# Kernel tuning notes

Hardware: AMD Instinct MI355X
Metric: run time of the kernel (lower is better)

Reference implementation:

```python
import jax, jax.numpy as jnp
import numpy as np

EMB = 512
GP = 128
NH = 8
HD = EMB // NH  # 64
B = 2
S = 1024


def _rel_shift(x):
    # Faithful port of DoubleAttentionLayer._rel_shift (pads dim 1, reinterprets
    # (B, J+1, K, n) as (J+1, B, K, n), drops first slice). Row-major reshape
    # semantics match torch .view on contiguous tensors exactly.
    Bsz, J, K, N = x.shape
    zp = jnp.zeros((Bsz, 1, K, N), x.dtype)
    xp = jnp.concatenate([zp, x], axis=1).reshape(J + 1, Bsz, K, N)
    return xp[1:].reshape(Bsz, J, K, N)


def _layernorm(x):
    # nn.LayerNorm(emb_dim, elementwise_affine=False), eps=1e-5
    m = jnp.mean(x, axis=-1, keepdims=True)
    v = jnp.var(x, axis=-1, keepdims=True)
    return (x - m) / jnp.sqrt(v + 1e-5)


def _attention(q, k, v, Bc, Bp, gpe, mask, Wp_w, Wp_b):
    Bsz, J, E = q.shape
    K = k.shape[1]
    # content scores
    qc = jnp.tanh((q + Bc).reshape(Bsz, J, NH, HD))
    kh = jnp.tanh(k.reshape(Bsz, K, NH, HD))
    ctx = jnp.einsum('bjnd,bknd->bjkn', qc, kh)
    # position scores (tanh before reshape in source for qp -- elementwise, same math)
    qp = jnp.tanh(q + Bp).reshape(Bsz, J, NH, HD)
    kp = jnp.tanh((gpe @ Wp_w + Wp_b).reshape(Bsz, -1, NH, HD))
    pos = jnp.einsum('bjnd,bknd->bjkn', qp, kp)
    pad = ctx.shape[2] - pos.shape[2]  # static; 0 in this configuration
    if pad > 0:
        # replicate-pad pos at front of k dim; constant(0)-pad mask (torch F.pad defaults)
        pos = jnp.concatenate([jnp.broadcast_to(pos[:, :, :1], (Bsz, J, pad, NH)), pos], axis=2)
        mask = jnp.concatenate([jnp.zeros(mask.shape[:2] + (pad, mask.shape[3]), mask.dtype), mask], axis=2)
    pos = _rel_shift(pos)
    att = (ctx + pos) / (HD ** 0.5) - 1e30 * mask
    att = jax.nn.softmax(att, axis=2)
    vh = jnp.tanh(v.reshape(Bsz, K, NH, HD))
    return jnp.einsum('bjkn,bknd->bjnd', att, vh).reshape(Bsz, J, E)


def setup_inputs() -> dict:
    key = jax.random.key(0)
    ks = jax.random.split(key, 12)
    u_emb = jax.random.normal(ks[0], (B, S, EMB), jnp.float32)
    f_emb = jax.random.normal(ks[1], (B, S, EMB), jnp.float32)
    gpe = jax.random.normal(ks[2], (B, S, GP), jnp.float32)
    # causal masks: 1 where attention is disallowed, broadcast over heads
    causal = (1.0 - jnp.tril(jnp.ones((S, S), jnp.float32)))[None, :, :, None]
    u_mask = jnp.broadcast_to(causal, (B, S, S, 1))
    f_mask = jnp.broadcast_to(causal, (B, S, S, 1))
    w = 0.02
    Wq_w = w * jax.random.normal(ks[3], (EMB, EMB), jnp.float32)
    Wq_b = jnp.zeros((EMB,), jnp.float32)
    Wkv_w = w * jax.random.normal(ks[4], (EMB, 2 * EMB), jnp.float32)
    Wkv_b = jnp.zeros((2 * EMB,), jnp.float32)
    Wp_w = w * jax.random.normal(ks[5], (GP, EMB), jnp.float32)
    Wp_b = jnp.zeros((EMB,), jnp.float32)
    Wu_w = w * jax.random.normal(ks[6], (EMB, EMB), jnp.float32)
    Wu_b = jnp.zeros((EMB,), jnp.float32)
    Bfc = 0.2 * jax.random.normal(ks[7], (1, 1, EMB), jnp.float32)
    Bfp = 0.2 * jax.random.normal(ks[8], (1, 1, EMB), jnp.float32)
    Buc = 0.2 * jax.random.normal(ks[9], (1, 1, EMB), jnp.float32)
    Bup = 0.2 * jax.random.normal(ks[10], (1, 1, EMB), jnp.float32)
    return {"u_emb": u_emb, "f_emb": f_emb, "gpe": gpe, "u_mask": u_mask, "f_mask": f_mask,
            "Wq_w": Wq_w, "Wq_b": Wq_b, "Wkv_w": Wkv_w, "Wkv_b": Wkv_b,
            "Wp_w": Wp_w, "Wp_b": Wp_b, "Wu_w": Wu_w, "Wu_b": Wu_b,
            "Bfc": Bfc, "Bfp": Bfp, "Buc": Buc, "Bup": Bup}


def reference(u_emb, f_emb, gpe, u_mask, f_mask, Wq_w, Wq_b, Wkv_w, Wkv_b,
              Wp_w, Wp_b, Wu_w, Wu_b, Bfc, Bfp, Buc, Bup):
    # first_part=True path: f_mem = f_emb (memory buffer registration has no output effect)
    q_u = f_emb @ Wu_w + Wu_b
    kv = f_emb @ Wkv_w + Wkv_b
    k, v = jnp.split(kv, 2, axis=-1)
    u_out = _layernorm(u_emb + _attention(q_u, k, v, Buc, Bup, gpe, u_mask, Wp_w, Wp_b))
    # last_layer=False: second attention over f stream
    q_f = f_emb @ Wq_w + Wq_b
    f_out = _layernorm(f_emb + _attention(q_f, k, v, Bfc, Bfp, gpe, f_mask, Wp_w, Wp_b))
    return (u_out, f_out)
```

## Files before the change

### kernel.cpp

```cpp
#include <hip/hip_runtime.h>
#include <math.h>

#define EMB 512
#define NH 8
#define HD 64
#define BB 2
#define SS 1024
#define ROWS (BB * SS)

typedef __attribute__((ext_vector_type(8))) short bhalf8;
typedef __attribute__((ext_vector_type(4))) float f32x4;
typedef __attribute__((ext_vector_type(8))) unsigned short us8;
typedef unsigned short ushort_t;

typedef const __attribute__((address_space(1))) void gas_void;
typedef __attribute__((address_space(3))) void las_void;

__device__ __forceinline__ void gl2lds16(const void* g, void* l) {
  __builtin_amdgcn_global_load_lds((gas_void*)g, (las_void*)l, 16, 0, 0);
}

__device__ __forceinline__ unsigned short f2bf(float x) {
  unsigned u = __float_as_uint(x);
  u = (u + 0x7FFFu + ((u >> 16) & 1u)) >> 16;
  return (unsigned short)u;
}
__device__ __forceinline__ float bf2f(unsigned short v) {
  return __uint_as_float(((unsigned)v) << 16);
}
__device__ __forceinline__ float fast_tanh(float x) {
  x = fminf(15.f, fmaxf(-15.f, x));
  const float e = __expf(2.f * x);
  return (e - 1.f) / (e + 1.f);
}

__global__ __launch_bounds__(256, 4) void projpe_kernel(
    const float* __restrict__ f_emb, const float* __restrict__ gpe,
    const float* __restrict__ Wu, const float* __restrict__ Wq,
    const float* __restrict__ Wkv, const float* __restrict__ Wp,
    const float* __restrict__ Wu_b, const float* __restrict__ Wq_b,
    const float* __restrict__ Wkv_b, const float* __restrict__ Wp_b,
    const float* __restrict__ Buc, const float* __restrict__ Bup,
    const float* __restrict__ Bfc, const float* __restrict__ Bfp,
    ushort_t* __restrict__ Qcomb, ushort_t* __restrict__ Kcomb,
    ushort_t* __restrict__ vhT, float* __restrict__ Onum,
    float* __restrict__ lpart) {
  const int bx = blockIdx.x;
  const int mb = blockIdx.y * 128;
  const int tid = threadIdx.x;
  const int w = tid >> 6, lane = tid & 63;
  const int ln = lane & 15, quad = lane >> 4;
  const int wm = (w >> 1) * 64, wn = (w & 1) * 32;

  __shared__ __align__(16) ushort_t sA[128 * 72];
  __shared__ __align__(16) ushort_t sB[64 * 72];

  const int fb = blockIdx.y * 40 + bx;
  if (fb < 512) {
    const float4 z4 = {0.f, 0.f, 0.f, 0.f};
#pragma unroll
    for (int i = 0; i < 4; ++i)
      ((float4*)Onum)[(size_t)fb * 1024 + i * 256 + tid] = z4;
  } else {
    lpart[(fb - 512) * 256 + tid] = 0.f;
  }
  if (fb == 0) {
    const int t2 = tid >> 7, rem = tid & 127;
    const int h = rem >> 4, d4 = (rem & 15) * 4;
    *(ushort4*)&Qcomb[((size_t)t2 * ROWS + 1023) * 1024 + h * 128 + 64 + d4] =
        make_ushort4(0, 0, 0, 0);
  }

  const bool isPe = (bx >= 32);
  const int nb = isPe ? 0 : bx * 64;
  const int npbase = isPe ? (bx - 32) * 64 : 0;
  const float* Af = isPe ? gpe : f_emb;
  const int lda = isPe ? 128 : 512;
  const int trips = isPe ? 2 : 8;

  const float* Wsrc;
  int Nw, coff;
  if (isPe) { Wsrc = Wp; Nw = 512; coff = npbase; }
  else if (nb < 512) { Wsrc = Wu; Nw = 512; coff = nb; }
  else if (nb < 1024) { Wsrc = Wq; Nw = 512; coff = nb - 512; }
  else { Wsrc = Wkv; Nw = 1024; coff = nb - 1024; }

  const int bn = tid & 63;
  const int bk0 = (tid >> 6) * 16;

  f32x4 acc[4][2];
#pragma unroll
  for (int rt = 0; rt < 4; ++rt)
#pragma unroll
    for (int ct = 0; ct < 2; ++ct) acc[rt][ct] = (f32x4){0.f, 0.f, 0.f, 0.f};

  float4 qa[8];
  float qbw[16];
#pragma unroll
  for (int i = 0; i < 4; ++i) {
    const int idx = tid + i * 256;
    const size_t base = (size_t)(mb + (idx >> 3)) * lda + (idx & 7) * 8;
    qa[2 * i] = *(const float4*)&Af[base];
    qa[2 * i + 1] = *(const float4*)&Af[base + 4];
  }
#pragma unroll
  for (int j = 0; j < 16; ++j)
    qbw[j] = Wsrc[(size_t)(bk0 + j) * Nw + coff + bn];

  for (int t0 = 0; t0 < trips; ++t0) {
    __syncthreads();
#pragma unroll
    for (int i = 0; i < 4; ++i) {
      const int idx = tid + i * 256;
      us8 o;
      const float4 a = qa[2 * i], b = qa[2 * i + 1];
      o[0] = f2bf(a.x); o[1] = f2bf(a.y); o[2] = f2bf(a.z); o[3] = f2bf(a.w);
      o[4] = f2bf(b.x); o[5] = f2bf(b.y); o[6] = f2bf(b.z); o[7] = f2bf(b.w);
      *(us8*)&sA[(idx >> 3) * 72 + (idx & 7) * 8] = o;
    }
    {
      us8 o0, o1;
#pragma unroll
      for (int j = 0; j < 8; ++j) {
        o0[j] = f2bf(qbw[j]);
        o1[j] = f2bf(qbw[8 + j]);
      }
      *(us8*)&sB[bn * 72 + bk0] = o0;
      *(us8*)&sB[bn * 72 + bk0 + 8] = o1;
    }
    __syncthreads();
    if (t0 < trips - 1) {
      const int k1 = (t0 + 1) * 64;
#pragma unroll
      for (int i = 0; i < 4; ++i) {
        const int idx = tid + i * 256;
        const size_t base = (size_t)(mb + (idx >> 3)) * lda + k1 + (idx & 7) * 8;
        qa[2 * i] = *(const float4*)&Af[base];
        qa[2 * i + 1] = *(const float4*)&Af[base + 4];
      }
#pragma unroll
      for (int j = 0; j < 16; ++j)
        qbw[j] = Wsrc[(size_t)(k1 + bk0 + j) * Nw + coff + bn];
    }
#pragma unroll
    for (int kc = 0; kc < 2; ++kc) {
      bhalf8 af[4], bf_[2];
#pragma unroll
      for (int rt = 0; rt < 4; ++rt)
        af[rt] =
            *(const bhalf8*)&sA[(wm + rt * 16 + ln) * 72 + kc * 32 + quad * 8];
#pragma unroll
      for (int ct = 0; ct < 2; ++ct)
        bf_[ct] =
            *(const bhalf8*)&sB[(wn + ct * 16 + ln) * 72 + kc * 32 + quad * 8];
#pragma unroll
      for (int rt = 0; rt < 4; ++rt)
#pragma unroll
        for (int ct = 0; ct < 2; ++ct)
          acc[rt][ct] = __builtin_amdgcn_mfma_f32_16x16x32_bf16(
              af[rt], bf_[ct], acc[rt][ct], 0, 0, 0);
    }
  }

  __syncthreads();
  ushort_t* sOut = sA;

  if (!isPe && nb >= 1536) {
#pragma unroll
    for (int ct = 0; ct < 2; ++ct) {
      const int nl = wn + ct * 16 + ln;
      const float wb = Wkv_b[nb + nl - 1024];
#pragma unroll
      for (int rt = 0; rt < 4; ++rt)
#pragma unroll
        for (int r = 0; r < 4; ++r) {
          const int ml = wm + rt * 16 + quad * 4 + r;
          sOut[nl * 136 + ml] = f2bf(fast_tanh(acc[rt][ct][r] + wb));
        }
    }
    __syncthreads();
    const int b = mb >> 10, mo = mb & 1023;
#pragma unroll
    for (int i = 0; i < 4; ++i) {
      const int idx = tid + i * 256;
      const int nl = idx >> 4, m8 = (idx & 15) * 8;
      const us8 v = *(const us8*)&sOut[nl * 136 + m8];
      *(us8*)&vhT[((size_t)b * 512 + (nb - 1536) + nl) * 1024 + mo + m8] = v;
    }
  } else {
    const float* WB =
        isPe ? Wp_b : (nb < 512 ? Wu_b : (nb < 1024 ? Wq_b : Wkv_b));
    const int woff =
        isPe ? npbase : (nb < 512 ? nb : (nb < 1024 ? nb - 512 : nb - 1024));
    const bool rawDump = (!isPe && nb < 1024);
#pragma unroll
    for (int ct = 0; ct < 2; ++ct) {
      const int nl = wn + ct * 16 + ln;
      const float wb = WB[woff + nl];
#pragma unroll
      for (int rt = 0; rt < 4; ++rt)
#pragma unroll
        for (int r = 0; r < 4; ++r) {
          const int ml = wm + rt * 16 + quad * 4 + r;
          const float v = acc[rt][ct][r] + wb;
          sOut[ml * 72 + nl] = f2bf(rawDump ? v : fast_tanh(v));
        }
    }
    __syncthreads();
#pragma unroll
    for (int i = 0; i < 4; ++i) {
      const int idx = tid + i * 256;
      const int rr = idx >> 3, c8 = (idx & 7) * 8;
      const int m = mb + rr;
      const us8 v = *(const us8*)&sOut[rr * 72 + c8];
      if (isPe) {
        const int n = npbase + c8;
        const int h = n >> 6;
        *(us8*)&Kcomb[(size_t)m * 1024 + h * 128 + 64 + (n & 63)] = v;
      } else if (nb < 1024) {
        const int strm = nb >= 512 ? 1 : 0;
        const int n = (nb - strm * 512) + c8;
        const int h = n >> 6;
        const float* BC = strm ? Bfc : Buc;
        const float* BP = strm ? Bfp : Bup;
        float bcA[8], bpA[8];
        *(float4*)&bcA[0] = *(const float4*)&BC[n];
        *(float4*)&bcA[4] = *(const float4*)&BC[n + 4];
        *(float4*)&bpA[0] = *(const float4*)&BP[n];
        *(float4*)&bpA[4] = *(const float4*)&BP[n + 4];
        us8 oc, op;
#pragma unroll
        for (int jj = 0; jj < 8; ++jj) {
          const float vv = bf2f((unsigned short)v[jj]);
          oc[jj] = f2bf(fast_tanh(vv + bcA[jj]));
          op[jj] = f2bf(fast_tanh(vv + bpA[jj]));
        }
        *(us8*)&Qcomb[((size_t)strm * ROWS + m) * 1024 + h * 128 + (n & 63)] =
            oc;
        if (m != 0) {
          const int mp = (m < 1024) ? m - 1 : m;
          *(us8*)&Qcomb[((size_t)strm * ROWS + mp) * 1024 + h * 128 + 64 +
                        (n & 63)] = op;
        }
      } else {
        const int n = (nb - 1024) + c8;
        const int h = n >> 6;
        *(us8*)&Kcomb[(size_t)m * 1024 + h * 128 + (n & 63)] = v;
      }
    }
  }
}

__global__ __launch_bounds__(256, 2) void attn_kernel(
    const ushort_t* __restrict__ Qcomb, const ushort_t* __restrict__ Kcomb,
    const ushort_t* __restrict__ vhT, float* __restrict__ Onum,
    float* __restrict__ lpart) {
  const int bid = blockIdx.x;
  const int tid = threadIdx.x;
  const int w = tid >> 6, lane = tid & 63;
  const int ln = lane & 15, quad = lane >> 4;

  __shared__ __align__(16) ushort_t sK[2 * 64 * 128];
  __shared__ __align__(16) ushort_t sV[2 * 64 * 64];
  __shared__ __align__(16) ushort_t sP[64 * 72];

  const int G0 = (bid * 17) >> 1;
  const int G1 = ((bid + 1) * 17) >> 1;
  const int cnt = G1 - G0;

  int c = G0 / 136;
  int u = G0 - c * 136;
  int jt = (int)((sqrtf(8.f * u + 1.f) - 1.f) * 0.5f);
  while ((jt + 1) * (jt + 2) / 2 <= u) ++jt;
  while (jt * (jt + 1) / 2 > u) --jt;
  int kt = u - jt * (jt + 1) / 2;
  int t = c >> 4, b = (c >> 3) & 1, h = c & 7;

  const int l4 = lane >> 4, p15 = lane & 15;
  const int l3 = lane >> 3, l7 = lane & 7;
#define STAGE_KV(B_, H_, KT_, BUF_)                                          \
  {                                                                          \
    const size_t kb_ = ((size_t)(B_)*SS + (KT_)*64) * 1024 + (H_)*128;       \
    ushort_t* bk_ = sK + (BUF_)*8192;                                        \
    _Pragma("unroll") for (int s_ = 0; s_ < 4; ++s_) {                       \
      const int q_ = w * 4 + s_;                                             \
      const int r_ = q_ * 4 + l4;                                            \
      const int gl_ = p15 ^ (r_ & 7);                                        \
      gl2lds16(&Kcomb[kb_ + (size_t)r_ * 1024 + gl_ * 8], &bk_[q_ * 512]);   \
    }                                                                        \
    const size_t vb_ = ((size_t)(B_)*512 + (H_)*64) * 1024 + (KT_)*64;       \
    ushort_t* bv_ = sV + (BUF_)*4096;                                        \
    _Pragma("unroll") for (int s_ = 0; s_ < 2; ++s_) {                       \
      const int q_ = w * 2 + s_;                                             \
      const int r_ = q_ * 8 + l3;                                            \
      const int gl_ = l7 ^ (r_ & 7);                                         \
      gl2lds16(&vhT[vb_ + (size_t)r_ * 1024 + gl_ * 8], &bv_[q_ * 512]);     \
    }                                                                        \
  }

  bhalf8 aq[4];
#define LOAD_AQ(T_, B_, H_, JT_)                                             \
  {                                                                          \
    const size_t qb_ =                                                       \
        ((size_t)(T_)*ROWS + (B_)*SS + (JT_)*64 + w * 16 + ln) * 1024 +      \
        (H_)*128 + quad * 8;                                                 \
    _Pragma("unroll") for (int kc_ = 0; kc_ < 4; ++kc_) aq[kc_] =            \
        *(const bhalf8*)&Qcomb[qb_ + kc_ * 32];                              \
  }

  STAGE_KV(b, h, kt, 0);
  LOAD_AQ(t, b, h, jt);

  f32x4 oacc[4];
#pragma unroll
  for (int ct = 0; ct < 4; ++ct) oacc[ct] = (f32x4){0.f, 0.f, 0.f, 0.f};
  float lsum[4] = {0.f, 0.f, 0.f, 0.f};

  for (int it = 0; it < cnt; ++it) {
    __syncthreads();
    const ushort_t* bK = sK + (it & 1) * 8192;
    const ushort_t* bV = sV + (it & 1) * 4096;

    int c2 = c, jt2 = jt, kt2 = kt + 1;
    if (kt2 > jt) {
      jt2 = jt + 1; kt2 = 0;
      if (jt2 > 15) { c2 = c + 1; jt2 = 0; }
    }
    if (it < cnt - 1) {
      const int b2 = (c2 >> 3) & 1, h2 = c2 & 7;
      STAGE_KV(b2, h2, kt2, ((it + 1) & 1));
    }

    f32x4 sacc[4];
#pragma unroll
    for (int ct = 0; ct < 4; ++ct) {
      sacc[ct] = (f32x4){0.f, 0.f, 0.f, 0.f};
#pragma unroll
      for (int kc = 0; kc < 4; ++kc) {
        const bhalf8 bk = *(const bhalf8*)&bK[(ct * 16 + ln) * 128 +
                                             (((kc * 4 + quad) ^ l7) << 3)];
        sacc[ct] = __builtin_amdgcn_mfma_f32_16x16x32_bf16(aq[kc], bk,
                                                           sacc[ct], 0, 0, 0);
      }
    }

    const bool diag = (kt == jt);
#pragma unroll
    for (int ct = 0; ct < 4; ++ct)
#pragma unroll
      for (int r = 0; r < 4; ++r) {
        float p;
        if (diag && (ct * 16 + ln > w * 16 + quad * 4 + r))
          p = 0.f;
        else
          p = __expf(sacc[ct][r] * 0.125f - 16.f);
        sacc[ct][r] = p;
        lsum[r] += p;
      }

#pragma unroll
    for (int ct = 0; ct < 4; ++ct)
#pragma unroll
      for (int r = 0; r < 4; ++r)
        sP[(w * 16 + quad * 4 + r) * 72 + ct * 16 + ln] =
            (ushort_t)(__float_as_uint(sacc[ct][r]) >> 16);

#pragma unroll
    for (int kc = 0; kc < 2; ++kc) {
      const bhalf8 ap =
          *(const bhalf8*)&sP[(w * 16 + ln) * 72 + kc * 32 + quad * 8];
#pragma unroll
      for (int ct = 0; ct < 4; ++ct) {
        const bhalf8 bv = *(const bhalf8*)&bV[(ct * 16 + ln) * 64 +
                                             (((kc * 4 + quad) ^ l7) << 3)];
        oacc[ct] = __builtin_amdgcn_mfma_f32_16x16x32_bf16(ap, bv, oacc[ct],
                                                           0, 0, 0);
      }
    }

    const bool rowEnd = (it == cnt - 1) || (jt2 != jt) || (c2 != c);
    if (rowEnd) {
#pragma unroll
      for (int r = 0; r < 4; ++r) {
        float s = lsum[r];
        s += __shfl_xor(s, 1);
        s += __shfl_xor(s, 2);
        s += __shfl_xor(s, 4);
        s += __shfl_xor(s, 8);
        const int j = jt * 64 + w * 16 + quad * 4 + r;
        if (ln == 0)
          atomicAdd(&lpart[((((t * 2 + b) << 10) + j) << 3) + h], s);
        const size_t orow = (((size_t)t * ROWS + b * SS + j) << 9) + h * 64;
#pragma unroll
        for (int ct = 0; ct < 4; ++ct)
          atomicAdd(&Onum[orow + ct * 16 + ln], oacc[ct][r]);
        lsum[r] = 0.f;
      }
#pragma unroll
      for (int ct = 0; ct < 4; ++ct) oacc[ct] = (f32x4){0.f, 0.f, 0.f, 0.f};
      if (it < cnt - 1) {
        const int t2 = c2 >> 4, b2 = (c2 >> 3) & 1, h2 = c2 & 7;
        LOAD_AQ(t2, b2, h2, jt2);
      }
    }
    c = c2; jt = jt2; kt = kt2;
    t = c >> 4; b = (c >> 3) & 1; h = c & 7;
  }
}

__global__ __launch_bounds__(256) void ln_kernel(
    const float* __restrict__ u_emb, const float* __restrict__ f_emb,
    const float* __restrict__ Onum, const float* __restrict__ lpart,
    float* __restrict__ out) {
  const int rid = blockIdx.x * 4 + (threadIdx.x >> 6);
  const int lane = threadIdx.x & 63;
  const int t = rid >> 11, row = rid & 2047;
  const int b = row >> 10, j = row & 1023;
  const float* resid = t ? f_emb : u_emb;
  const size_t base = (size_t)row * 512;
  const size_t obase = ((size_t)t * ROWS + row) * 512;
  const int o = lane * 8;
  const int h = lane >> 3;
  const float inv = 1.f / lpart[((((t * 2 + b) << 10) + j) << 3) + h];

  const float4 n0 = *(const float4*)&Onum[obase + o];
  const float4 n1 = *(const float4*)&Onum[obase + o + 4];
  const float4 r0 = *(const float4*)&resid[base + o];
  const float4 r1 = *(const float4*)&resid[base + o + 4];
  float y[8];
  y[0] = r0.x + n0.x * inv; y[1] = r0.y + n0.y * inv;
  y[2] = r0.z + n0.z * inv; y[3] = r0.w + n0.w * inv;
  y[4] = r1.x + n1.x * inv; y[5] = r1.y + n1.y * inv;
  y[6] = r1.z + n1.z * inv; y[7] = r1.w + n1.w * inv;

  float s = 0.f, q = 0.f;
#pragma unroll
  for (int i = 0; i < 8; ++i) {
    s += y[i];
    q += y[i] * y[i];
  }
#pragma unroll
  for (int off = 1; off < 64; off <<= 1) {
    s += __shfl_xor(s, off);
    q += __shfl_xor(q, off);
  }
  const float mean = s * (1.f / 512.f);
  const float var = q * (1.f / 512.f) - mean * mean;
  const float rstd = rsqrtf(var + 1e-5f);

  float4 o0, o1;
  o0.x = (y[0] - mean) * rstd; o0.y = (y[1] - mean) * rstd;
  o0.z = (y[2] - mean) * rstd; o0.w = (y[3] - mean) * rstd;
  o1.x = (y[4] - mean) * rstd; o1.y = (y[5] - mean) * rstd;
  o1.z = (y[6] - mean) * rstd; o1.w = (y[7] - mean) * rstd;
  *(float4*)&out[obase + o] = o0;
  *(float4*)&out[obase + o + 4] = o1;
}

extern "C" void kernel_launch(void* const* d_in, const int* in_sizes, int n_in,
                              void* d_out, int out_size, void* d_ws,
                              size_t ws_size, hipStream_t stream) {
  (void)in_sizes; (void)n_in; (void)out_size; (void)ws_size;
  const float* u_emb = (const float*)d_in[0];
  const float* f_emb = (const float*)d_in[1];
  const float* gpe = (const float*)d_in[2];
  const float* Wq_w = (const float*)d_in[5];
  const float* Wq_b = (const float*)d_in[6];
  const float* Wkv_w = (const float*)d_in[7];
  const float* Wkv_b = (const float*)d_in[8];
  const float* Wp_w = (const float*)d_in[9];
  const float* Wp_b = (const float*)d_in[10];
  const float* Wu_w = (const float*)d_in[11];
  const float* Wu_b = (const float*)d_in[12];
  const float* Bfc = (const float*)d_in[13];
  const float* Bfp = (const float*)d_in[14];
  const float* Buc = (const float*)d_in[15];
  const float* Bup = (const float*)d_in[16];
  float* out = (float*)d_out;

  ushort_t* ws = (ushort_t*)d_ws;
  const size_t SZ = (size_t)ROWS * EMB;
  ushort_t* Qcomb = ws;
  ushort_t* Kcomb = ws + 4 * SZ;
  ushort_t* vhT = ws + 6 * SZ;
  float* Onum = (float*)(ws + 7 * SZ);
  float* lpart = (float*)(ws + 11 * SZ);

  dim3 blk(256);
  hipLaunchKernelGGL(projpe_kernel, dim3(40, 16), blk, 0, stream, f_emb, gpe,
                     Wu_w, Wq_w, Wkv_w, Wp_w, Wu_b, Wq_b, Wkv_b, Wp_b, Buc,
                     Bup, Bfc, Bfp, Qcomb, Kcomb, vhT, Onum, lpart);
  hipLaunchKernelGGL(attn_kernel, dim3(512), blk, 0, stream, Qcomb, Kcomb, vhT,
                     Onum, lpart);
  hipLaunchKernelGGL(ln_kernel, dim3(1024), blk, 0, stream, u_emb, f_emb, Onum,
                     lpart, out);
}
```

Baseline: 158.2 us.

## Share K/V tiles across both attention streams and retile projection GEMM

The attention kernel now processes both query streams (u and f) against each staged K/V tile, so each tile is loaded once and reused for two score/PV passes, halving the number of work items per block schedule. The projection kernel switches to 64-row tiles with a doubled grid, double-buffered shared memory and a single barrier per k-step to raise occupancy and overlap loads. The change costs more registers in the attention kernel from the doubled accumulators and Q fragments, and the zero-init indexing is reworked to fit the new grid.

```diff
diff --git a/kernel.cpp b/kernel.cpp
--- a/kernel.cpp
+++ b/kernel.cpp
@@ -46,25 +46,24 @@
     ushort_t* __restrict__ vhT, float* __restrict__ Onum,
     float* __restrict__ lpart) {
   const int bx = blockIdx.x;
-  const int mb = blockIdx.y * 128;
+  const int mb = blockIdx.y * 64;
   const int tid = threadIdx.x;
   const int w = tid >> 6, lane = tid & 63;
   const int ln = lane & 15, quad = lane >> 4;
-  const int wm = (w >> 1) * 64, wn = (w & 1) * 32;
-
-  __shared__ __align__(16) ushort_t sA[128 * 72];
-  __shared__ __align__(16) ushort_t sB[64 * 72];
+  const int wm = w * 16;
+
+  __shared__ __align__(16) ushort_t sA[2 * 64 * 72];
+  __shared__ __align__(16) ushort_t sB[2 * 64 * 72];
 
   const int fb = blockIdx.y * 40 + bx;
-  if (fb < 512) {
+  if (fb < 1024) {
     const float4 z4 = {0.f, 0.f, 0.f, 0.f};
 #pragma unroll
-    for (int i = 0; i < 4; ++i)
-      ((float4*)Onum)[(size_t)fb * 1024 + i * 256 + tid] = z4;
-  } else {
-    lpart[(fb - 512) * 256 + tid] = 0.f;
-  }
-  if (fb == 0) {
+    for (int i = 0; i < 2; ++i)
+      ((float4*)Onum)[(size_t)fb * 512 + i * 256 + tid] = z4;
+  } else if (fb < 1152) {
+    lpart[(fb - 1024) * 256 + tid] = 0.f;
+  } else if (fb == 1152) {
     const int t2 = tid >> 7, rem = tid & 127;
     const int h = rem >> 4, d4 = (rem & 15) * 4;
     *(ushort4*)&Qcomb[((size_t)t2 * ROWS + 1023) * 1024 + h * 128 + 64 + d4] =
@@ -85,80 +84,67 @@
   else if (nb < 1024) { Wsrc = Wq; Nw = 512; coff = nb - 512; }
   else { Wsrc = Wkv; Nw = 1024; coff = nb - 1024; }
 
-  const int bn = tid & 63;
-  const int bk0 = (tid >> 6) * 16;
-
-  f32x4 acc[4][2];
-#pragma unroll
-  for (int rt = 0; rt < 4; ++rt)
-#pragma unroll
-    for (int ct = 0; ct < 2; ++ct) acc[rt][ct] = (f32x4){0.f, 0.f, 0.f, 0.f};
-
-  float4 qa[8];
+  const int arow = tid >> 2, ac16 = (tid & 3) * 16;
+  const int bn = tid & 63, bk0 = (tid >> 6) * 16;
+
+  f32x4 acc[4];
+#pragma unroll
+  for (int ct = 0; ct < 4; ++ct) acc[ct] = (f32x4){0.f, 0.f, 0.f, 0.f};
+
+  float4 qa[4];
   float qbw[16];
 #pragma unroll
-  for (int i = 0; i < 4; ++i) {
-    const int idx = tid + i * 256;
-    const size_t base = (size_t)(mb + (idx >> 3)) * lda + (idx & 7) * 8;
-    qa[2 * i] = *(const float4*)&Af[base];
-    qa[2 * i + 1] = *(const float4*)&Af[base + 4];
-  }
+  for (int i = 0; i < 4; ++i)
+    qa[i] = *(const float4*)&Af[(size_t)(mb + arow) * lda + ac16 + i * 4];
 #pragma unroll
   for (int j = 0; j < 16; ++j)
     qbw[j] = Wsrc[(size_t)(bk0 + j) * Nw + coff + bn];
 
   for (int t0 = 0; t0 < trips; ++t0) {
-    __syncthreads();
-#pragma unroll
-    for (int i = 0; i < 4; ++i) {
-      const int idx = tid + i * 256;
-      us8 o;
-      const float4 a = qa[2 * i], b = qa[2 * i + 1];
-      o[0] = f2bf(a.x); o[1] = f2bf(a.y); o[2] = f2bf(a.z); o[3] = f2bf(a.w);
-      o[4] = f2bf(b.x); o[5] = f2bf(b.y); o[6] = f2bf(b.z); o[7] = f2bf(b.w);
-      *(us8*)&sA[(idx >> 3) * 72 + (idx & 7) * 8] = o;
-    }
+    ushort_t* bA = sA + (t0 & 1) * 4608;
+    ushort_t* bB = sB + (t0 & 1) * 4608;
     {
       us8 o0, o1;
 #pragma unroll
+      for (int j = 0; j < 4; ++j) {
+        o0[j] = f2bf(((const float*)&qa[0])[j]);
+        o0[4 + j] = f2bf(((const float*)&qa[1])[j]);
+        o1[j] = f2bf(((const float*)&qa[2])[j]);
+        o1[4 + j] = f2bf(((const float*)&qa[3])[j]);
+      }
+      *(us8*)&bA[arow * 72 + ac16] = o0;
+      *(us8*)&bA[arow * 72 + ac16 + 8] = o1;
+      us8 b0, b1;
+#pragma unroll
       for (int j = 0; j < 8; ++j) {
-        o0[j] = f2bf(qbw[j]);
-        o1[j] = f2bf(qbw[8 + j]);
-      }
-      *(us8*)&sB[bn * 72 + bk0] = o0;
-      *(us8*)&sB[bn * 72 + bk0 + 8] = o1;
-    }
-    __syncthreads();
+        b0[j] = f2bf(qbw[j]);
+        b1[j] = f2bf(qbw[8 + j]);
+      }
+      *(us8*)&bB[bn * 72 + bk0] = b0;
+      *(us8*)&bB[bn * 72 + bk0 + 8] = b1;
+    }
     if (t0 < trips - 1) {
       const int k1 = (t0 + 1) * 64;
 #pragma unroll
-      for (int i = 0; i < 4; ++i) {
-        const int idx = tid + i * 256;
-        const size_t base = (size_t)(mb + (idx >> 3)) * lda + k1 + (idx & 7) * 8;
-        qa[2 * i] = *(const float4*)&Af[base];
-        qa[2 * i + 1] = *(const float4*)&Af[base + 4];
-      }
+      for (int i = 0; i < 4; ++i)
+        qa[i] =
+            *(const float4*)&Af[(size_t)(mb + arow) * lda + k1 + ac16 + i * 4];
 #pragma unroll
       for (int j = 0; j < 16; ++j)
         qbw[j] = Wsrc[(size_t)(k1 + bk0 + j) * Nw + coff + bn];
     }
+    __syncthreads();
 #pragma unroll
     for (int kc = 0; kc < 2; ++kc) {
-      bhalf8 af[4], bf_[2];
-#pragma unroll
-      for (int rt = 0; rt < 4; ++rt)
-        af[rt] =
-            *(const bhalf8*)&sA[(wm + rt * 16 + ln) * 72 + kc * 32 + quad * 8];
-#pragma unroll
-      for (int ct = 0; ct < 2; ++ct)
-        bf_[ct] =
-            *(const bhalf8*)&sB[(wn + ct * 16 + ln) * 72 + kc * 32 + quad * 8];
-#pragma unroll
-      for (int rt = 0; rt < 4; ++rt)
-#pragma unroll
-        for (int ct = 0; ct < 2; ++ct)
-          acc[rt][ct] = __builtin_amdgcn_mfma_f32_16x16x32_bf16(
-              af[rt], bf_[ct], acc[rt][ct], 0, 0, 0);
+      const bhalf8 af =
+          *(const bhalf8*)&bA[(wm + ln) * 72 + kc * 32 + quad * 8];
+#pragma unroll
+      for (int ct = 0; ct < 4; ++ct) {
+        const bhalf8 bf_ =
+            *(const bhalf8*)&bB[(ct * 16 + ln) * 72 + kc * 32 + quad * 8];
+        acc[ct] =
+            __builtin_amdgcn_mfma_f32_16x16x32_bf16(af, bf_, acc[ct], 0, 0, 0);
+      }
     }
   }
 
@@ -167,23 +153,21 @@
 
   if (!isPe && nb >= 1536) {
 #pragma unroll
-    for (int ct = 0; ct < 2; ++ct) {
-      const int nl = wn + ct * 16 + ln;
+    for (int ct = 0; ct < 4; ++ct) {
+      const int nl = ct * 16 + ln;
       const float wb = Wkv_b[nb + nl - 1024];
 #pragma unroll
-      for (int rt = 0; rt < 4; ++rt)
-#pragma unroll
-        for (int r = 0; r < 4; ++r) {
-          const int ml = wm + rt * 16 + quad * 4 + r;
-          sOut[nl * 136 + ml] = f2bf(fast_tanh(acc[rt][ct][r] + wb));
-        }
+      for (int r = 0; r < 4; ++r) {
+        const int ml = wm + quad * 4 + r;
+        sOut[nl * 136 + ml] = f2bf(fast_tanh(acc[ct][r] + wb));
+      }
     }
     __syncthreads();
     const int b = mb >> 10, mo = mb & 1023;
 #pragma unroll
-    for (int i = 0; i < 4; ++i) {
+    for (int i = 0; i < 2; ++i) {
       const int idx = tid + i * 256;
-      const int nl = idx >> 4, m8 = (idx & 15) * 8;
+      const int nl = idx >> 3, m8 = (idx & 7) * 8;
       const us8 v = *(const us8*)&sOut[nl * 136 + m8];
       *(us8*)&vhT[((size_t)b * 512 + (nb - 1536) + nl) * 1024 + mo + m8] = v;
     }
@@ -194,21 +178,19 @@
         isPe ? npbase : (nb < 512 ? nb : (nb < 1024 ? nb - 512 : nb - 1024));
     const bool rawDump = (!isPe && nb < 1024);
 #pragma unroll
-    for (int ct = 0; ct < 2; ++ct) {
-      const int nl = wn + ct * 16 + ln;
+    for (int ct = 0; ct < 4; ++ct) {
+      const int nl = ct * 16 + ln;
       const float wb = WB[woff + nl];
 #pragma unroll
-      for (int rt = 0; rt < 4; ++rt)
-#pragma unroll
-        for (int r = 0; r < 4; ++r) {
-          const int ml = wm + rt * 16 + quad * 4 + r;
-          const float v = acc[rt][ct][r] + wb;
-          sOut[ml * 72 + nl] = f2bf(rawDump ? v : fast_tanh(v));
-        }
+      for (int r = 0; r < 4; ++r) {
+        const int ml = wm + quad * 4 + r;
+        const float v = acc[ct][r] + wb;
+        sOut[ml * 72 + nl] = f2bf(rawDump ? v : fast_tanh(v));
+      }
     }
     __syncthreads();
 #pragma unroll
-    for (int i = 0; i < 4; ++i) {
+    for (int i = 0; i < 2; ++i) {
       const int idx = tid + i * 256;
       const int rr = idx >> 3, c8 = (idx & 7) * 8;
       const int m = mb + rr;
@@ -264,8 +246,8 @@
   __shared__ __align__(16) ushort_t sV[2 * 64 * 64];
   __shared__ __align__(16) ushort_t sP[64 * 72];
 
-  const int G0 = (bid * 17) >> 1;
-  const int G1 = ((bid + 1) * 17) >> 1;
+  const int G0 = (bid * 17) >> 2;
+  const int G1 = ((bid + 1) * 17) >> 2;
   const int cnt = G1 - G0;
 
   int c = G0 / 136;
@@ -274,7 +256,7 @@
   while ((jt + 1) * (jt + 2) / 2 <= u) ++jt;
   while (jt * (jt + 1) / 2 > u) --jt;
   int kt = u - jt * (jt + 1) / 2;
-  int t = c >> 4, b = (c >> 3) & 1, h = c & 7;
+  int b = c >> 3, h = c & 7;
 
   const int l4 = lane >> 4, p15 = lane & 15;
   const int l3 = lane >> 3, l7 = lane & 7;
@@ -298,23 +280,27 @@
     }                                                                        \
   }
 
-  bhalf8 aq[4];
-#define LOAD_AQ(T_, B_, H_, JT_)                                             \
+  bhalf8 aq[2][4];
+#define LOAD_AQ2(B_, H_, JT_)                                                \
   {                                                                          \
-    const size_t qb_ =                                                       \
-        ((size_t)(T_)*ROWS + (B_)*SS + (JT_)*64 + w * 16 + ln) * 1024 +      \
-        (H_)*128 + quad * 8;                                                 \
-    _Pragma("unroll") for (int kc_ = 0; kc_ < 4; ++kc_) aq[kc_] =            \
-        *(const bhalf8*)&Qcomb[qb_ + kc_ * 32];                              \
+    _Pragma("unroll") for (int t_ = 0; t_ < 2; ++t_) {                       \
+      const size_t qb_ =                                                     \
+          ((size_t)t_ * ROWS + (B_)*SS + (JT_)*64 + w * 16 + ln) * 1024 +    \
+          (H_)*128 + quad * 8;                                               \
+      _Pragma("unroll") for (int kc_ = 0; kc_ < 4; ++kc_) aq[t_][kc_] =      \
+          *(const bhalf8*)&Qcomb[qb_ + kc_ * 32];                            \
+    }                                                                        \
   }
 
   STAGE_KV(b, h, kt, 0);
-  LOAD_AQ(t, b, h, jt);
-
-  f32x4 oacc[4];
-#pragma unroll
-  for (int ct = 0; ct < 4; ++ct) oacc[ct] = (f32x4){0.f, 0.f, 0.f, 0.f};
-  float lsum[4] = {0.f, 0.f, 0.f, 0.f};
+  LOAD_AQ2(b, h, jt);
+
+  f32x4 oacc[2][4];
+#pragma unroll
+  for (int ts = 0; ts < 2; ++ts)
+#pragma unroll
+    for (int ct = 0; ct < 4; ++ct) oacc[ts][ct] = (f32x4){0.f, 0.f, 0.f, 0.f};
+  float lsum[2][4] = {{0.f, 0.f, 0.f, 0.f}, {0.f, 0.f, 0.f, 0.f}};
 
   for (int it = 0; it < cnt; ++it) {
     __syncthreads();
@@ -331,80 +317,82 @@
       STAGE_KV(b2, h2, kt2, ((it + 1) & 1));
     }
 
-    f32x4 sacc[4];
-#pragma unroll
-    for (int ct = 0; ct < 4; ++ct) {
-      sacc[ct] = (f32x4){0.f, 0.f, 0.f, 0.f};
-#pragma unroll
-      for (int kc = 0; kc < 4; ++kc) {
-        const bhalf8 bk = *(const bhalf8*)&bK[(ct * 16 + ln) * 128 +
-                                             (((kc * 4 + quad) ^ l7) << 3)];
-        sacc[ct] = __builtin_amdgcn_mfma_f32_16x16x32_bf16(aq[kc], bk,
-                                                           sacc[ct], 0, 0, 0);
-      }
-    }
-
     const bool diag = (kt == jt);
 #pragma unroll
-    for (int ct = 0; ct < 4; ++ct)
-#pragma unroll
-      for (int r = 0; r < 4; ++r) {
-        float p;
-        if (diag && (ct * 16 + ln > w * 16 + quad * 4 + r))
-          p = 0.f;
-        else
-          p = __expf(sacc[ct][r] * 0.125f - 16.f);
-        sacc[ct][r] = p;
-        lsum[r] += p;
-      }
-
-#pragma unroll
-    for (int ct = 0; ct < 4; ++ct)
-#pragma unroll
-      for (int r = 0; r < 4; ++r)
-        sP[(w * 16 + quad * 4 + r) * 72 + ct * 16 + ln] =
-            (ushort_t)(__float_as_uint(sacc[ct][r]) >> 16);
-
-#pragma unroll
-    for (int kc = 0; kc < 2; ++kc) {
-      const bhalf8 ap =
-          *(const bhalf8*)&sP[(w * 16 + ln) * 72 + kc * 32 + quad * 8];
+    for (int ts = 0; ts < 2; ++ts) {
+      f32x4 sacc[4];
 #pragma unroll
       for (int ct = 0; ct < 4; ++ct) {
-        const bhalf8 bv = *(const bhalf8*)&bV[(ct * 16 + ln) * 64 +
-                                             (((kc * 4 + quad) ^ l7) << 3)];
-        oacc[ct] = __builtin_amdgcn_mfma_f32_16x16x32_bf16(ap, bv, oacc[ct],
-                                                           0, 0, 0);
+        sacc[ct] = (f32x4){0.f, 0.f, 0.f, 0.f};
+#pragma unroll
+        for (int kc = 0; kc < 4; ++kc) {
+          const bhalf8 bk = *(const bhalf8*)&bK[(ct * 16 + ln) * 128 +
+                                               (((kc * 4 + quad) ^ l7) << 3)];
+          sacc[ct] = __builtin_amdgcn_mfma_f32_16x16x32_bf16(aq[ts][kc], bk,
+                                                             sacc[ct], 0, 0, 0);
+        }
+      }
+#pragma unroll
+      for (int ct = 0; ct < 4; ++ct)
+#pragma unroll
+        for (int r = 0; r < 4; ++r) {
+          float p;
+          if (diag && (ct * 16 + ln > w * 16 + quad * 4 + r))
+            p = 0.f;
+          else
+            p = __expf(sacc[ct][r] * 0.125f - 16.f);
+          sacc[ct][r] = p;
+          lsum[ts][r] += p;
+        }
+#pragma unroll
+      for (int ct = 0; ct < 4; ++ct)
+#pragma unroll
+        for (int r = 0; r < 4; ++r)
+          sP[(w * 16 + quad * 4 + r) * 72 + ct * 16 + ln] =
+              (ushort_t)(__float_as_uint(sacc[ct][r]) >> 16);
+#pragma unroll
+      for (int kc = 0; kc < 2; ++kc) {
+        const bhalf8 ap =
+            *(const bhalf8*)&sP[(w * 16 + ln) * 72 + kc * 32 + quad * 8];
+#pragma unroll
+        for (int ct = 0; ct < 4; ++ct) {
+          const bhalf8 bv = *(const bhalf8*)&bV[(ct * 16 + ln) * 64 +
+                                                (((kc * 4 + quad) ^ l7) << 3)];
+          oacc[ts][ct] = __builtin_amdgcn_mfma_f32_16x16x32_bf16(
+              ap, bv, oacc[ts][ct], 0, 0, 0);
+        }
       }
     }
 
     const bool rowEnd = (it == cnt - 1) || (jt2 != jt) || (c2 != c);
     if (rowEnd) {
 #pragma unroll
-      for (int r = 0; r < 4; ++r) {
-        float s = lsum[r];
-        s += __shfl_xor(s, 1);
-        s += __shfl_xor(s, 2);
-        s += __shfl_xor(s, 4);
-        s += __shfl_xor(s, 8);
-        const int j = jt * 64 + w * 16 + quad * 4 + r;
-        if (ln == 0)
-          atomicAdd(&lpart[((((t * 2 + b) << 10) + j) << 3) + h], s);
-        const size_t orow = (((size_t)t * ROWS + b * SS + j) << 9) + h * 64;
-#pragma unroll
-        for (int ct = 0; ct < 4; ++ct)
-          atomicAdd(&Onum[orow + ct * 16 + ln], oacc[ct][r]);
-        lsum[r] = 0.f;
-      }
-#pragma unroll
-      for (int ct = 0; ct < 4; ++ct) oacc[ct] = (f32x4){0.f, 0.f, 0.f, 0.f};
+      for (int ts = 0; ts < 2; ++ts)
+#pragma unroll
+        for (int r = 0; r < 4; ++r) {
+          float s = lsum[ts][r];
+          s += __shfl_xor(s, 1);
+          s += __shfl_xor(s, 2);
+          s += __shfl_xor(s, 4);
+          s += __shfl_xor(s, 8);
+          const int j = jt * 64 + w * 16 + quad * 4 + r;
+          if (ln == 0)
+            atomicAdd(&lpart[((((ts * 2 + b) << 10) + j) << 3) + h], s);
+          const size_t orow = (((size_t)ts * ROWS + b * SS + j) << 9) + h * 64;
+#pragma unroll
+          for (int ct = 0; ct < 4; ++ct)
+            atomicAdd(&Onum[orow + ct * 16 + ln], oacc[ts][ct][r]);
+          lsum[ts][r] = 0.f;
+#pragma unroll
+          for (int ct = 0; ct < 4; ++ct) oacc[ts][ct][r] = 0.f;
+        }
       if (it < cnt - 1) {
-        const int t2 = c2 >> 4, b2 = (c2 >> 3) & 1, h2 = c2 & 7;
-        LOAD_AQ(t2, b2, h2, jt2);
+        const int b2 = (c2 >> 3) & 1, h2 = c2 & 7;
+        LOAD_AQ2(b2, h2, jt2);
       }
     }
     c = c2; jt = jt2; kt = kt2;
-    t = c >> 4; b = (c >> 3) & 1; h = c & 7;
+    b = c >> 3; h = c & 7;
   }
 }
 
@@ -487,7 +475,7 @@
   float* lpart = (float*)(ws + 11 * SZ);
 
   dim3 blk(256);
-  hipLaunchKernelGGL(projpe_kernel, dim3(40, 16), blk, 0, stream, f_emb, gpe,
+  hipLaunchKernelGGL(projpe_kernel, dim3(40, 32), blk, 0, stream, f_emb, gpe,
                      Wu_w, Wq_w, Wkv_w, Wp_w, Wu_b, Wq_b, Wkv_b, Wp_b, Buc,
                      Bup, Bfc, Bfp, Qcomb, Kcomb, vhT, Onum, lpart);
   hipLaunchKernelGGL(attn_kernel, dim3(512), blk, 0, stream, Qcomb, Kcomb, vhT,
```

New measurement: 167.6 us. +6.0%, slower.

## Process both attention streams per K/V tile to share staged K and V

Applied to the files above, without the earlier changes.

Each attention block now handles the u and f query streams together against the same staged K/V tile, holding two sets of Q fragments and accumulators. Work units are halved (16 combos of batch and head instead of 32), so each K/V tile is loaded into LDS once and reused for both streams. This cuts global-to-LDS traffic and the number of work items, at the cost of more registers, which may lower occupancy, and a serial dependency through the shared sP buffer between the two streams.

```diff
diff --git a/kernel.cpp b/kernel.cpp
--- a/kernel.cpp
+++ b/kernel.cpp
@@ -264,8 +264,8 @@
   __shared__ __align__(16) ushort_t sV[2 * 64 * 64];
   __shared__ __align__(16) ushort_t sP[64 * 72];
 
-  const int G0 = (bid * 17) >> 1;
-  const int G1 = ((bid + 1) * 17) >> 1;
+  const int G0 = (bid * 17) >> 2;
+  const int G1 = ((bid + 1) * 17) >> 2;
   const int cnt = G1 - G0;
 
   int c = G0 / 136;
@@ -274,7 +274,7 @@
   while ((jt + 1) * (jt + 2) / 2 <= u) ++jt;
   while (jt * (jt + 1) / 2 > u) --jt;
   int kt = u - jt * (jt + 1) / 2;
-  int t = c >> 4, b = (c >> 3) & 1, h = c & 7;
+  int b = c >> 3, h = c & 7;
 
   const int l4 = lane >> 4, p15 = lane & 15;
   const int l3 = lane >> 3, l7 = lane & 7;
@@ -298,23 +298,27 @@
     }                                                                        \
   }
 
-  bhalf8 aq[4];
-#define LOAD_AQ(T_, B_, H_, JT_)                                             \
+  bhalf8 aq[2][4];
+#define LOAD_AQ2(B_, H_, JT_)                                                \
   {                                                                          \
-    const size_t qb_ =                                                       \
-        ((size_t)(T_)*ROWS + (B_)*SS + (JT_)*64 + w * 16 + ln) * 1024 +      \
-        (H_)*128 + quad * 8;                                                 \
-    _Pragma("unroll") for (int kc_ = 0; kc_ < 4; ++kc_) aq[kc_] =            \
-        *(const bhalf8*)&Qcomb[qb_ + kc_ * 32];                              \
+    _Pragma("unroll") for (int t_ = 0; t_ < 2; ++t_) {                       \
+      const size_t qb_ =                                                     \
+          ((size_t)t_ * ROWS + (B_)*SS + (JT_)*64 + w * 16 + ln) * 1024 +    \
+          (H_)*128 + quad * 8;                                               \
+      _Pragma("unroll") for (int kc_ = 0; kc_ < 4; ++kc_) aq[t_][kc_] =      \
+          *(const bhalf8*)&Qcomb[qb_ + kc_ * 32];                            \
+    }                                                                        \
   }
 
   STAGE_KV(b, h, kt, 0);
-  LOAD_AQ(t, b, h, jt);
-
-  f32x4 oacc[4];
-#pragma unroll
-  for (int ct = 0; ct < 4; ++ct) oacc[ct] = (f32x4){0.f, 0.f, 0.f, 0.f};
-  float lsum[4] = {0.f, 0.f, 0.f, 0.f};
+  LOAD_AQ2(b, h, jt);
+
+  f32x4 oacc[2][4];
+#pragma unroll
+  for (int ts = 0; ts < 2; ++ts)
+#pragma unroll
+    for (int ct = 0; ct < 4; ++ct) oacc[ts][ct] = (f32x4){0.f, 0.f, 0.f, 0.f};
+  float lsum[2][4] = {{0.f, 0.f, 0.f, 0.f}, {0.f, 0.f, 0.f, 0.f}};
 
   for (int it = 0; it < cnt; ++it) {
     __syncthreads();
@@ -331,80 +335,82 @@
       STAGE_KV(b2, h2, kt2, ((it + 1) & 1));
     }
 
-    f32x4 sacc[4];
-#pragma unroll
-    for (int ct = 0; ct < 4; ++ct) {
-      sacc[ct] = (f32x4){0.f, 0.f, 0.f, 0.f};
-#pragma unroll
-      for (int kc = 0; kc < 4; ++kc) {
-        const bhalf8 bk = *(const bhalf8*)&bK[(ct * 16 + ln) * 128 +
-                                             (((kc * 4 + quad) ^ l7) << 3)];
-        sacc[ct] = __builtin_amdgcn_mfma_f32_16x16x32_bf16(aq[kc], bk,
-                                                           sacc[ct], 0, 0, 0);
+    const bool diag = (kt == jt);
+#pragma unroll
+    for (int ts = 0; ts < 2; ++ts) {
+      f32x4 sacc[4];
+#pragma unroll
+      for (int ct = 0; ct < 4; ++ct) {
+        sacc[ct] = (f32x4){0.f, 0.f, 0.f, 0.f};
+#pragma unroll
+        for (int kc = 0; kc < 4; ++kc) {
+          const bhalf8 bk = *(const bhalf8*)&bK[(ct * 16 + ln) * 128 +
+                                               (((kc * 4 + quad) ^ l7) << 3)];
+          sacc[ct] = __builtin_amdgcn_mfma_f32_16x16x32_bf16(aq[ts][kc], bk,
+                                                             sacc[ct], 0, 0, 0);
+        }
       }
-    }
-
-    const bool diag = (kt == jt);
-#pragma unroll
-    for (int ct = 0; ct < 4; ++ct)
-#pragma unroll
-      for (int r = 0; r < 4; ++r) {
-        float p;
-        if (diag && (ct * 16 + ln > w * 16 + quad * 4 + r))
-          p = 0.f;
-        else
-          p = __expf(sacc[ct][r] * 0.125f - 16.f);
-        sacc[ct][r] = p;
-        lsum[r] += p;
-      }
-
-#pragma unroll
-    for (int ct = 0; ct < 4; ++ct)
-#pragma unroll
-      for (int r = 0; r < 4; ++r)
-        sP[(w * 16 + quad * 4 + r) * 72 + ct * 16 + ln] =
-            (ushort_t)(__float_as_uint(sacc[ct][r]) >> 16);
-
-#pragma unroll
-    for (int kc = 0; kc < 2; ++kc) {
-      const bhalf8 ap =
-          *(const bhalf8*)&sP[(w * 16 + ln) * 72 + kc * 32 + quad * 8];
-#pragma unroll
-      for (int ct = 0; ct < 4; ++ct) {
-        const bhalf8 bv = *(const bhalf8*)&bV[(ct * 16 + ln) * 64 +
-                                             (((kc * 4 + quad) ^ l7) << 3)];
-        oacc[ct] = __builtin_amdgcn_mfma_f32_16x16x32_bf16(ap, bv, oacc[ct],
-                                                           0, 0, 0);
+#pragma unroll
+      for (int ct = 0; ct < 4; ++ct)
+#pragma unroll
+        for (int r = 0; r < 4; ++r) {
+          float p;
+          if (diag && (ct * 16 + ln > w * 16 + quad * 4 + r))
+            p = 0.f;
+          else
+            p = __expf(sacc[ct][r] * 0.125f - 16.f);
+          sacc[ct][r] = p;
+          lsum[ts][r] += p;
+        }
+#pragma unroll
+      for (int ct = 0; ct < 4; ++ct)
+#pragma unroll
+        for (int r = 0; r < 4; ++r)
+          sP[(w * 16 + quad * 4 + r) * 72 + ct * 16 + ln] =
+              (ushort_t)(__float_as_uint(sacc[ct][r]) >> 16);
+#pragma unroll
+      for (int kc = 0; kc < 2; ++kc) {
+        const bhalf8 ap =
+            *(const bhalf8*)&sP[(w * 16 + ln) * 72 + kc * 32 + quad * 8];
+#pragma unroll
+        for (int ct = 0; ct < 4; ++ct) {
+          const bhalf8 bv = *(const bhalf8*)&bV[(ct * 16 + ln) * 64 +
+                                                (((kc * 4 + quad) ^ l7) << 3)];
+          oacc[ts][ct] = __builtin_amdgcn_mfma_f32_16x16x32_bf16(
+              ap, bv, oacc[ts][ct], 0, 0, 0);
+        }
       }
     }
 
     const bool rowEnd = (it == cnt - 1) || (jt2 != jt) || (c2 != c);
     if (rowEnd) {
 #pragma unroll
-      for (int r = 0; r < 4; ++r) {
-        float s = lsum[r];
-        s += __shfl_xor(s, 1);
-        s += __shfl_xor(s, 2);
-        s += __shfl_xor(s, 4);
-        s += __shfl_xor(s, 8);
-        const int j = jt * 64 + w * 16 + quad * 4 + r;
-        if (ln == 0)
-          atomicAdd(&lpart[((((t * 2 + b) << 10) + j) << 3) + h], s);
-        const size_t orow = (((size_t)t * ROWS + b * SS + j) << 9) + h * 64;
-#pragma unroll
-        for (int ct = 0; ct < 4; ++ct)
-          atomicAdd(&Onum[orow + ct * 16 + ln], oacc[ct][r]);
-        lsum[r] = 0.f;
+      for (int ts = 0; ts < 2; ++ts)
+#pragma unroll
+        for (int r = 0; r < 4; ++r) {
+          float s = lsum[ts][r];
+          s += __shfl_xor(s, 1);
+          s += __shfl_xor(s, 2);
+          s += __shfl_xor(s, 4);
+          s += __shfl_xor(s, 8);
+          const int j = jt * 64 + w * 16 + quad * 4 + r;
+          if (ln == 0)
+            atomicAdd(&lpart[((((ts * 2 + b) << 10) + j) << 3) + h], s);
+          const size_t orow = (((size_t)ts * ROWS + b * SS + j) << 9) + h * 64;
+#pragma unroll
+          for (int ct = 0; ct < 4; ++ct)
+            atomicAdd(&Onum[orow + ct * 16 + ln], oacc[ts][ct][r]);
+          lsum[ts][r] = 0.f;
+#pragma unroll
+          for (int ct = 0; ct < 4; ++ct) oacc[ts][ct][r] = 0.f;
+        }
+      if (it < cnt - 1) {
+        const int b2 = (c2 >> 3) & 1, h2 = c2 & 7;
+        LOAD_AQ2(b2, h2, jt2);
       }
-#pragma unroll
-      for (int ct = 0; ct < 4; ++ct) oacc[ct] = (f32x4){0.f, 0.f, 0.f, 0.f};
-      if (it < cnt - 1) {
-        const int t2 = c2 >> 4, b2 = (c2 >> 3) & 1, h2 = c2 & 7;
-        LOAD_AQ(t2, b2, h2, jt2);
-      }
     }
     c = c2; jt = jt2; kt = kt2;
-    t = c >> 4; b = (c >> 3) & 1; h = c & 7;
+    b = c >> 3; h = c & 7;
   }
 }
 
```

Result: slower. 166.2 us (+5.1%).
